# Optimization experiments

Measured on AMD Instinct MI355X. Metric: run time of the kernel, lower is better.

Reference implementation:

```python
import jax, jax.numpy as jnp
import numpy as np

NEG_BIG = -9e15
ALPHA = 0.2  # leaky relu slope

def setup_inputs() -> dict:
    key = jax.random.key(0)
    k1, k2, k3, k4, k5 = jax.random.split(key, 5)
    N, F_in, F_out, H = 4096, 512, 64, 8
    x = jax.random.normal(k1, (N, F_in), dtype=jnp.float32)
    adj = jax.random.randint(k2, (N, N), 0, 2, dtype=jnp.int32)
    W = jax.random.normal(k3, (H, F_in, F_out), dtype=jnp.float32) * (1.414 * (2.0 / (F_in + F_out)) ** 0.5)
    a_source = jax.random.normal(k4, (H, 1, F_out), dtype=jnp.float32) * (1.414 * (2.0 / (1 + F_out)) ** 0.5)
    a_target = jax.random.normal(k5, (H, 1, F_out), dtype=jnp.float32) * (1.414 * (2.0 / (1 + F_out)) ** 0.5)
    return {"x": x, "adj": adj, "W": W, "a_source": a_source, "a_target": a_target}

def reference(x, adj, W, a_source, a_target):
    # Wh: [H, N, F_out]
    Wh = jnp.einsum('nf,hfo->hno', x, W)
    # additive attention logits
    s_i = jnp.sum(a_source * Wh, axis=2, keepdims=True)          # [H, N, 1]
    s_j = jnp.sum(a_target * Wh, axis=2, keepdims=True)          # [H, N, 1]
    e = s_i + jnp.swapaxes(s_j, 1, 2)                            # [H, N, N]
    e = jnp.where(e > 0, e, ALPHA * e)                           # leaky relu
    e = jnp.where(adj[None] > 0, e, jnp.float32(NEG_BIG))        # adjacency mask
    attention = jax.nn.softmax(e, axis=2)                        # [H, N, N]
    h_prime = jnp.einsum('hij,hjo->hio', attention, Wh)          # [H, N, F_out]
    return h_prime
```

## Files before the change

### kernel.cpp

```cpp
#include <hip/hip_runtime.h>
#include <hip/hip_fp16.h>
#include <cstdint>

#define N_NODES 4096
#define F_IN    512
#define F_OUT   64
#define H_HEADS 8
#define JC      4

constexpr float L2E = 1.44269504088896f;

typedef _Float16 half2_t __attribute__((ext_vector_type(2)));
typedef _Float16 half4_t __attribute__((ext_vector_type(4)));
typedef _Float16 half8_t __attribute__((ext_vector_type(8)));
typedef float    f32x4   __attribute__((ext_vector_type(4)));

__device__ inline unsigned int exp2_pk_u(unsigned int au) {
    __half2 h = __builtin_bit_cast(__half2, au);
    h = h2exp2(h);
    return __builtin_bit_cast(unsigned int, h);
}

__global__ __launch_bounds__(256) void k_prep(const int* __restrict__ adj,
                                              const float* __restrict__ W,
                                              unsigned long long* __restrict__ adjwT,
                                              _Float16* __restrict__ wfrag) {
    if (blockIdx.x < 128) {
        int gid = blockIdx.x * 256 + threadIdx.x;
        int h     = gid >> 12;
        int kt    = (gid >> 8) & 15;
        int ntile = (gid >> 6) & 3;
        int lane  = gid & 63;
        int c0 = lane & 15, g = lane >> 4;
        const float* src = W + ((size_t)h * F_IN + kt * 32 + 8 * g) * F_OUT + ntile * 16 + c0;
        half8_t hv;
        #pragma unroll
        for (int t = 0; t < 8; t++) hv[t] = (_Float16)src[(size_t)t * F_OUT];
        *reinterpret_cast<half8_t*>(&wfrag[(size_t)gid * 8]) = hv;
        return;
    }
    int bid  = blockIdx.x - 128;
    int lane = threadIdx.x & 63;
    int wid  = (int)((bid * 256 + threadIdx.x) >> 6);
    int nwaves = (2048 * 256) >> 6;
    const int nchunks = N_NODES * (N_NODES / 64);
    for (int cf = wid; cf < nchunks; cf += nwaves) {
        int v = adj[(size_t)cf * 64 + lane];
        unsigned long long mask = __ballot(v > 0);
        if (lane == 0) {
            int i = cf >> 6, c = cf & 63;
            adjwT[(size_t)c * N_NODES + i] = mask;
        }
    }
}

__global__ __launch_bounds__(512) void k_wh_mfma(const float* __restrict__ x,
                                                 const _Float16* __restrict__ wfrag,
                                                 const float* __restrict__ a_src,
                                                 const float* __restrict__ a_tgt,
                                                 _Float16* __restrict__ WhFrag,
                                                 float* __restrict__ s_iL,
                                                 _Float16* __restrict__ s_jLh) {
    __shared__ f32x4 red[4][4][64];
    const int h    = blockIdx.y;
    const int rt   = blockIdx.x;
    const int t    = threadIdx.x;
    const int lane = t & 63;
    const int w    = t >> 6;
    const int mtw  = w & 3;
    const int kh   = w >> 2;
    const int mt   = rt * 4 + mtw;
    const int c0   = lane & 15;
    const int gl   = lane >> 4;

    f32x4 acc0 = {0.f, 0.f, 0.f, 0.f};
    f32x4 acc1 = {0.f, 0.f, 0.f, 0.f};
    f32x4 acc2 = {0.f, 0.f, 0.f, 0.f};
    f32x4 acc3 = {0.f, 0.f, 0.f, 0.f};

    const float* __restrict__ xr = x + (size_t)(mt * 16 + c0) * F_IN + 8 * gl + kh * 256;
    const _Float16* __restrict__ Bf = wfrag + (size_t)h * (16 * 4 * 512)
                                    + (size_t)kh * 8 * 2048 + (size_t)lane * 8;

    #pragma unroll
    for (int kt = 0; kt < 8; kt++) {
        float4 v0 = *reinterpret_cast<const float4*>(xr + kt * 32);
        float4 v1 = *reinterpret_cast<const float4*>(xr + kt * 32 + 4);
        half8_t a;
        a[0] = (_Float16)v0.x; a[1] = (_Float16)v0.y; a[2] = (_Float16)v0.z; a[3] = (_Float16)v0.w;
        a[4] = (_Float16)v1.x; a[5] = (_Float16)v1.y; a[6] = (_Float16)v1.z; a[7] = (_Float16)v1.w;
        const _Float16* Bk = Bf + (size_t)kt * 2048;
        half8_t b0 = *reinterpret_cast<const half8_t*>(Bk);
        half8_t b1 = *reinterpret_cast<const half8_t*>(Bk + 512);
        half8_t b2 = *reinterpret_cast<const half8_t*>(Bk + 1024);
        half8_t b3 = *reinterpret_cast<const half8_t*>(Bk + 1536);
        acc0 = __builtin_amdgcn_mfma_f32_16x16x32_f16(a, b0, acc0, 0, 0, 0);
        acc1 = __builtin_amdgcn_mfma_f32_16x16x32_f16(a, b1, acc1, 0, 0, 0);
        acc2 = __builtin_amdgcn_mfma_f32_16x16x32_f16(a, b2, acc2, 0, 0, 0);
        acc3 = __builtin_amdgcn_mfma_f32_16x16x32_f16(a, b3, acc3, 0, 0, 0);
    }

    if (kh == 1) {
        red[mtw][0][lane] = acc0;
        red[mtw][1][lane] = acc1;
        red[mtw][2][lane] = acc2;
        red[mtw][3][lane] = acc3;
    }
    __syncthreads();
    if (kh == 1) return;

    acc0 += red[mtw][0][lane];
    acc1 += red[mtw][1][lane];
    acc2 += red[mtw][2][lane];
    acc3 += red[mtw][3][lane];

    const float as0 = a_src[h * 64 + c0],      at0 = a_tgt[h * 64 + c0];
    const float as1 = a_src[h * 64 + 16 + c0], at1 = a_tgt[h * 64 + 16 + c0];
    const float as2 = a_src[h * 64 + 32 + c0], at2 = a_tgt[h * 64 + 32 + c0];
    const float as3 = a_src[h * 64 + 48 + c0], at3 = a_tgt[h * 64 + 48 + c0];

    #pragma unroll
    for (int reg = 0; reg < 4; reg++) {
        float vi = acc0[reg] * as0 + acc1[reg] * as1 + acc2[reg] * as2 + acc3[reg] * as3;
        float vj = acc0[reg] * at0 + acc1[reg] * at1 + acc2[reg] * at2 + acc3[reg] * at3;
        #pragma unroll
        for (int mm = 8; mm >= 1; mm >>= 1) {
            vi += __shfl_xor(vi, mm, 64);
            vj += __shfl_xor(vj, mm, 64);
        }
        if (c0 == 0) {
            int row = mt * 16 + 4 * gl + reg;
            s_iL[h * N_NODES + row]  = vi * L2E;
            s_jLh[h * N_NODES + row] = (_Float16)(vj * L2E);
        }
    }

    const int cc    = mt >> 2;
    const int kb    = (mt >> 1) & 1;
    const int lanep = c0 + 16 * ((mt & 1) * 2 + (gl >> 1));
    const int tb    = 4 * (gl & 1);
    _Float16* dst = WhFrag + (size_t)h * (N_NODES * 64)
                  + (size_t)(cc * 2 + kb) * 2048 + (size_t)lanep * 8 + tb;
    f32x4 accs[4] = {acc0, acc1, acc2, acc3};
    #pragma unroll
    for (int ot = 0; ot < 4; ot++) {
        half4_t hv;
        #pragma unroll
        for (int reg = 0; reg < 4; reg++) hv[reg] = (_Float16)accs[ot][reg];
        *reinterpret_cast<half4_t*>(dst + ot * 512) = hv;
    }
}

__global__ __launch_bounds__(256) void k_hmax(const _Float16* __restrict__ s_jLh,
                                              float* __restrict__ mxAll) {
    __shared__ float red[4];
    const int h = blockIdx.x;
    const int t = threadIdx.x;
    const _Float16* p = s_jLh + h * N_NODES;
    float m = -INFINITY;
    for (int k = t; k < N_NODES; k += 256) m = fmaxf(m, (float)p[k]);
    #pragma unroll
    for (int mm = 32; mm >= 1; mm >>= 1) m = fmaxf(m, __shfl_xor(m, mm, 64));
    if ((t & 63) == 0) red[t >> 6] = m;
    __syncthreads();
    if (t == 0) mxAll[h] = fmaxf(fmaxf(red[0], red[1]), fmaxf(red[2], red[3]));
}

__global__ __launch_bounds__(256) void k_attn_mfma(const _Float16* __restrict__ WhFrag,
                                                   const float* __restrict__ s_iL,
                                                   const float* __restrict__ mxAll,
                                                   const _Float16* __restrict__ s_jLh,
                                                   const unsigned long long* __restrict__ adjwT,
                                                   float* __restrict__ out0,
                                                   _Float16* __restrict__ partH,
                                                   float* __restrict__ lbuf) {
    __shared__ unsigned int ktab[256][4];
    __shared__ _Float16 Bs[2][4096];
    {
        unsigned int bm = threadIdx.x;
        #pragma unroll
        for (int q = 0; q < 4; q++) {
            unsigned int lo = ((bm >> (2 * q)) & 1u) ? 0xFFFFu : 0u;
            unsigned int hi = ((bm >> (2 * q + 1)) & 1u) ? 0xFFFF0000u : 0u;
            ktab[bm][q] = lo | hi;
        }
    }

    const int tid  = threadIdx.x;
    const int h    = blockIdx.y;
    const int jc   = blockIdx.z;
    const int lane = tid & 63;
    const int w    = tid >> 6;
    const int i0   = blockIdx.x * 64 + w * 16;
    const int mrow = lane & 15;
    const int gl   = lane >> 4;
    const int gl8  = gl << 3;

    const float siL = s_iL[h * N_NODES + i0 + mrow];
    const float tmx = siL + mxAll[h];
    const float m   = fmaxf(tmx, 0.2f * tmx);
    const _Float16 uh  = (_Float16)(siL - m);
    const _Float16 n8h = (_Float16)(-0.8f * m);
    half8_t u8, n88, c028;
    #pragma unroll
    for (int q = 0; q < 8; q++) { u8[q] = uh; n88[q] = n8h; c028[q] = (_Float16)0.2f; }

    const _Float16* __restrict__ sjh = s_jLh + h * N_NODES;
    const _Float16* __restrict__ Bh  = WhFrag + (size_t)h * (N_NODES * 64);

    half8_t vone;
    #pragma unroll
    for (int q = 0; q < 8; q++) vone[q] = (_Float16)1.0f;

    f32x4 acc0 = {0.f, 0.f, 0.f, 0.f};
    f32x4 acc1 = {0.f, 0.f, 0.f, 0.f};
    f32x4 acc2 = {0.f, 0.f, 0.f, 0.f};
    f32x4 acc3 = {0.f, 0.f, 0.f, 0.f};
    f32x4 accl = {0.f, 0.f, 0.f, 0.f};

    const int NC   = (N_NODES / 64) / JC;
    const int cbeg = jc * NC;
    const int cend = cbeg + NC;

    {
        const _Float16* src = Bh + (size_t)cbeg * 4096 + tid * 8;
        *reinterpret_cast<half8_t*>(&Bs[0][tid * 8])        = *reinterpret_cast<const half8_t*>(src);
        *reinterpret_cast<half8_t*>(&Bs[0][2048 + tid * 8]) = *reinterpret_cast<const half8_t*>(src + 2048);
    }
    __syncthreads();

    int cur = 0;
    for (int c = cbeg; c < cend; c++) {
        half8_t n0, n1;
        const bool hasNext = (c + 1 < cend);
        if (hasNext) {
            const _Float16* src = Bh + (size_t)(c + 1) * 4096 + tid * 8;
            n0 = *reinterpret_cast<const half8_t*>(src);
            n1 = *reinterpret_cast<const half8_t*>(src + 2048);
        }

        uint2 word = *reinterpret_cast<const uint2*>(&adjwT[(size_t)c * N_NODES + i0 + mrow]);
        #pragma unroll
        for (int kb = 0; kb < 2; kb++) {
            const int jb = c * 64 + kb * 32 + 8 * gl;
            half8_t sjv = *reinterpret_cast<const half8_t*>(&sjh[jb]);
            unsigned int bm8 = ((kb ? word.y : word.x) >> gl8) & 0xFFu;
            uint4 mk = *reinterpret_cast<const uint4*>(&ktab[bm8][0]);

            half8_t a1v = u8 + sjv;
            half8_t a2v = a1v * c028 + n88;
            half8_t amv = __builtin_elementwise_max(a1v, a2v);
            uint4 amu = __builtin_bit_cast(uint4, amv);
            uint4 pu;
            pu.x = exp2_pk_u(amu.x) & mk.x;
            pu.y = exp2_pk_u(amu.y) & mk.y;
            pu.z = exp2_pk_u(amu.z) & mk.z;
            pu.w = exp2_pk_u(amu.w) & mk.w;
            half8_t af = __builtin_bit_cast(half8_t, pu);

            const _Float16* Bk = &Bs[cur][kb * 2048 + lane * 8];
            half8_t b0 = *reinterpret_cast<const half8_t*>(Bk);
            half8_t b1 = *reinterpret_cast<const half8_t*>(Bk + 512);
            half8_t b2 = *reinterpret_cast<const half8_t*>(Bk + 1024);
            half8_t b3 = *reinterpret_cast<const half8_t*>(Bk + 1536);

            acc0 = __builtin_amdgcn_mfma_f32_16x16x32_f16(af, b0, acc0, 0, 0, 0);
            acc1 = __builtin_amdgcn_mfma_f32_16x16x32_f16(af, b1, acc1, 0, 0, 0);
            acc2 = __builtin_amdgcn_mfma_f32_16x16x32_f16(af, b2, acc2, 0, 0, 0);
            acc3 = __builtin_amdgcn_mfma_f32_16x16x32_f16(af, b3, acc3, 0, 0, 0);
            accl = __builtin_amdgcn_mfma_f32_16x16x32_f16(af, vone, accl, 0, 0, 0);
        }

        if (hasNext) {
            *reinterpret_cast<half8_t*>(&Bs[cur ^ 1][tid * 8])        = n0;
            *reinterpret_cast<half8_t*>(&Bs[cur ^ 1][2048 + tid * 8]) = n1;
        }
        __syncthreads();
        cur ^= 1;
    }

    float* lp = lbuf + (size_t)jc * (H_HEADS * N_NODES);
    if (mrow == 0) {
        #pragma unroll
        for (int r = 0; r < 4; r++)
            lp[h * N_NODES + i0 + 4 * gl + r] = accl[r];
    }
    if (jc == 0) {
        #pragma unroll
        for (int r = 0; r < 4; r++) {
            int row   = i0 + 4 * gl + r;
            size_t ob = ((size_t)h * N_NODES + row) * 64 + mrow;
            out0[ob + 0]  = acc0[r];
            out0[ob + 16] = acc1[r];
            out0[ob + 32] = acc2[r];
            out0[ob + 48] = acc3[r];
        }
    } else {
        _Float16* op = partH + (size_t)(jc - 1) * ((size_t)H_HEADS * N_NODES * F_OUT);
        #pragma unroll
        for (int r = 0; r < 4; r++) {
            int row   = i0 + 4 * gl + r;
            size_t ob = ((size_t)h * N_NODES + row) * 64 + mrow;
            op[ob + 0]  = (_Float16)acc0[r];
            op[ob + 16] = (_Float16)acc1[r];
            op[ob + 32] = (_Float16)acc2[r];
            op[ob + 48] = (_Float16)acc3[r];
        }
    }
}

__global__ __launch_bounds__(256) void k_norm(float* __restrict__ out,
                                              const _Float16* __restrict__ partH,
                                              const float* __restrict__ lbuf) {
    const int HN = H_HEADS * N_NODES;
    int idx = blockIdx.x * 256 + threadIdx.x;
    int row = idx >> 4;
    float inv = 1.0f / (lbuf[row] + lbuf[HN + row] + lbuf[2 * HN + row] + lbuf[3 * HN + row]);
    float4 a = reinterpret_cast<const float4*>(out)[idx];
    float s0 = a.x, s1 = a.y, s2 = a.z, s3 = a.w;
    #pragma unroll
    for (int p = 0; p < 3; p++) {
        half4_t hp = *reinterpret_cast<const half4_t*>(
            &partH[(size_t)p * ((size_t)H_HEADS * N_NODES * F_OUT) + (size_t)idx * 4]);
        s0 += (float)hp[0]; s1 += (float)hp[1]; s2 += (float)hp[2]; s3 += (float)hp[3];
    }
    float4 v = {s0 * inv, s1 * inv, s2 * inv, s3 * inv};
    reinterpret_cast<float4*>(out)[idx] = v;
}

extern "C" void kernel_launch(void* const* d_in, const int* in_sizes, int n_in,
                              void* d_out, int out_size, void* d_ws, size_t ws_size,
                              hipStream_t stream) {
    const float* x     = (const float*)d_in[0];
    const int*   adj   = (const int*)d_in[1];
    const float* W     = (const float*)d_in[2];
    const float* a_src = (const float*)d_in[3];
    const float* a_tgt = (const float*)d_in[4];
    float* out = (float*)d_out;

    char* ws = (char*)d_ws;
    size_t off = 0;
    auto alloc = [&](size_t bytes) -> char* {
        char* p = ws + off;
        off += (bytes + 255) & ~(size_t)255;
        return p;
    };
    _Float16* WhFrag = (_Float16*)alloc((size_t)H_HEADS * N_NODES * F_OUT * 2);
    _Float16* wfrag  = (_Float16*)alloc((size_t)H_HEADS * 16 * 4 * 64 * 8 * 2);
    float* s_iL      = (float*)alloc((size_t)H_HEADS * N_NODES * 4);
    _Float16* s_jLh  = (_Float16*)alloc((size_t)H_HEADS * N_NODES * 2);
    float* mxAll     = (float*)alloc((size_t)H_HEADS * 4);
    float* lbuf      = (float*)alloc((size_t)JC * H_HEADS * N_NODES * 4);
    _Float16* partH  = (_Float16*)alloc((size_t)(JC - 1) * H_HEADS * N_NODES * F_OUT * 2);
    unsigned long long* adjwT = (unsigned long long*)alloc((size_t)N_NODES * (N_NODES / 64) * 8);
    (void)ws_size;

    k_prep<<<2176, 256, 0, stream>>>(adj, W, adjwT, wfrag);
    k_wh_mfma<<<dim3(N_NODES / 64, H_HEADS), 512, 0, stream>>>(x, wfrag, a_src, a_tgt,
                                                               WhFrag, s_iL, s_jLh);
    k_hmax<<<H_HEADS, 256, 0, stream>>>(s_jLh, mxAll);
    k_attn_mfma<<<dim3(N_NODES / 64, H_HEADS, JC), 256, 0, stream>>>(WhFrag, s_iL, mxAll, s_jLh,
                                                                     adjwT, out, partH, lbuf);
    k_norm<<<(H_HEADS * N_NODES * F_OUT / 4) / 256, 256, 0, stream>>>(out, partH, lbuf);
}
```

Measured before the change: 82.58 us.

## Process two 16-row tiles per wave in attention kernel to reuse B fragments

Each wave now covers 32 query rows instead of 16. Every shared-memory B fragment load and every s_j load therefore feeds two sets of MFMAs, and the grid is halved in x. This cuts LDS traffic and the per-block staging overhead for each row. The cost is doubled accumulator registers, so a launch_bounds occupancy hint of 4 is added, and there are fewer blocks (1024) to fill the GPU.

```diff
diff --git a/kernel.cpp b/kernel.cpp
--- a/kernel.cpp
+++ b/kernel.cpp
@@ -166,14 +166,14 @@
     if (t == 0) mxAll[h] = fmaxf(fmaxf(red[0], red[1]), fmaxf(red[2], red[3]));
 }
 
-__global__ __launch_bounds__(256) void k_attn_mfma(const _Float16* __restrict__ WhFrag,
-                                                   const float* __restrict__ s_iL,
-                                                   const float* __restrict__ mxAll,
-                                                   const _Float16* __restrict__ s_jLh,
-                                                   const unsigned long long* __restrict__ adjwT,
-                                                   float* __restrict__ out0,
-                                                   _Float16* __restrict__ partH,
-                                                   float* __restrict__ lbuf) {
+__global__ __launch_bounds__(256, 4) void k_attn_mfma(const _Float16* __restrict__ WhFrag,
+                                                      const float* __restrict__ s_iL,
+                                                      const float* __restrict__ mxAll,
+                                                      const _Float16* __restrict__ s_jLh,
+                                                      const unsigned long long* __restrict__ adjwT,
+                                                      float* __restrict__ out0,
+                                                      _Float16* __restrict__ partH,
+                                                      float* __restrict__ lbuf) {
     __shared__ unsigned int ktab[256][4];
     __shared__ _Float16 Bs[2][4096];
     {
@@ -191,19 +191,22 @@
     const int jc   = blockIdx.z;
     const int lane = tid & 63;
     const int w    = tid >> 6;
-    const int i0   = blockIdx.x * 64 + w * 16;
+    const int i0   = blockIdx.x * 128 + w * 32;
     const int mrow = lane & 15;
     const int gl   = lane >> 4;
     const int gl8  = gl << 3;
 
-    const float siL = s_iL[h * N_NODES + i0 + mrow];
-    const float tmx = siL + mxAll[h];
-    const float m   = fmaxf(tmx, 0.2f * tmx);
-    const _Float16 uh  = (_Float16)(siL - m);
-    const _Float16 n8h = (_Float16)(-0.8f * m);
-    half8_t u8, n88, c028;
-    #pragma unroll
-    for (int q = 0; q < 8; q++) { u8[q] = uh; n88[q] = n8h; c028[q] = (_Float16)0.2f; }
+    const float siL0 = s_iL[h * N_NODES + i0 + mrow];
+    const float siL1 = s_iL[h * N_NODES + i0 + 16 + mrow];
+    const float mxh  = mxAll[h];
+    const float tm0 = siL0 + mxh, tm1 = siL1 + mxh;
+    const float m0 = fmaxf(tm0, 0.2f * tm0);
+    const float m1 = fmaxf(tm1, 0.2f * tm1);
+    const half2_t u2_0 = {(_Float16)(siL0 - m0), (_Float16)(siL0 - m0)};
+    const half2_t u2_1 = {(_Float16)(siL1 - m1), (_Float16)(siL1 - m1)};
+    const half2_t n82_0 = {(_Float16)(-0.8f * m0), (_Float16)(-0.8f * m0)};
+    const half2_t n82_1 = {(_Float16)(-0.8f * m1), (_Float16)(-0.8f * m1)};
+    const half2_t c02 = {(_Float16)0.2f, (_Float16)0.2f};
 
     const _Float16* __restrict__ sjh = s_jLh + h * N_NODES;
     const _Float16* __restrict__ Bh  = WhFrag + (size_t)h * (N_NODES * 64);
@@ -212,11 +215,9 @@
     #pragma unroll
     for (int q = 0; q < 8; q++) vone[q] = (_Float16)1.0f;
 
-    f32x4 acc0 = {0.f, 0.f, 0.f, 0.f};
-    f32x4 acc1 = {0.f, 0.f, 0.f, 0.f};
-    f32x4 acc2 = {0.f, 0.f, 0.f, 0.f};
-    f32x4 acc3 = {0.f, 0.f, 0.f, 0.f};
-    f32x4 accl = {0.f, 0.f, 0.f, 0.f};
+    f32x4 accA0 = {0,0,0,0}, accA1 = {0,0,0,0}, accA2 = {0,0,0,0}, accA3 = {0,0,0,0};
+    f32x4 accB0 = {0,0,0,0}, accB1 = {0,0,0,0}, accB2 = {0,0,0,0}, accB3 = {0,0,0,0};
+    f32x4 acclA = {0,0,0,0}, acclB = {0,0,0,0};
 
     const int NC   = (N_NODES / 64) / JC;
     const int cbeg = jc * NC;
@@ -239,36 +240,57 @@
             n1 = *reinterpret_cast<const half8_t*>(src + 2048);
         }
 
-        uint2 word = *reinterpret_cast<const uint2*>(&adjwT[(size_t)c * N_NODES + i0 + mrow]);
+        uint2 word0 = *reinterpret_cast<const uint2*>(&adjwT[(size_t)c * N_NODES + i0 + mrow]);
+        uint2 word1 = *reinterpret_cast<const uint2*>(&adjwT[(size_t)c * N_NODES + i0 + 16 + mrow]);
+
         #pragma unroll
         for (int kb = 0; kb < 2; kb++) {
             const int jb = c * 64 + kb * 32 + 8 * gl;
             half8_t sjv = *reinterpret_cast<const half8_t*>(&sjh[jb]);
-            unsigned int bm8 = ((kb ? word.y : word.x) >> gl8) & 0xFFu;
-            uint4 mk = *reinterpret_cast<const uint4*>(&ktab[bm8][0]);
-
-            half8_t a1v = u8 + sjv;
-            half8_t a2v = a1v * c028 + n88;
-            half8_t amv = __builtin_elementwise_max(a1v, a2v);
-            uint4 amu = __builtin_bit_cast(uint4, amv);
-            uint4 pu;
-            pu.x = exp2_pk_u(amu.x) & mk.x;
-            pu.y = exp2_pk_u(amu.y) & mk.y;
-            pu.z = exp2_pk_u(amu.z) & mk.z;
-            pu.w = exp2_pk_u(amu.w) & mk.w;
-            half8_t af = __builtin_bit_cast(half8_t, pu);
+            unsigned int bm0 = ((kb ? word0.y : word0.x) >> gl8) & 0xFFu;
+            unsigned int bm1 = ((kb ? word1.y : word1.x) >> gl8) & 0xFFu;
+            uint4 mk0 = *reinterpret_cast<const uint4*>(&ktab[bm0][0]);
+            uint4 mk1 = *reinterpret_cast<const uint4*>(&ktab[bm1][0]);
+
+            uint4 sju = __builtin_bit_cast(uint4, sjv);
+            uint4 p0u, p1u;
+            #pragma unroll
+            for (int q = 0; q < 4; q++) {
+                unsigned int sw = (q == 0) ? sju.x : (q == 1) ? sju.y : (q == 2) ? sju.z : sju.w;
+                half2_t sj2 = __builtin_bit_cast(half2_t, sw);
+                half2_t a1 = u2_0 + sj2;
+                half2_t am = __builtin_elementwise_max(a1, a1 * c02 + n82_0);
+                unsigned int pa = exp2_pk_u(__builtin_bit_cast(unsigned int, am));
+                half2_t b1 = u2_1 + sj2;
+                half2_t bm = __builtin_elementwise_max(b1, b1 * c02 + n82_1);
+                unsigned int pb = exp2_pk_u(__builtin_bit_cast(unsigned int, bm));
+                unsigned int ka = (q == 0) ? mk0.x : (q == 1) ? mk0.y : (q == 2) ? mk0.z : mk0.w;
+                unsigned int kbm = (q == 0) ? mk1.x : (q == 1) ? mk1.y : (q == 2) ? mk1.z : mk1.w;
+                pa &= ka; pb &= kbm;
+                if (q == 0) { p0u.x = pa; p1u.x = pb; }
+                else if (q == 1) { p0u.y = pa; p1u.y = pb; }
+                else if (q == 2) { p0u.z = pa; p1u.z = pb; }
+                else { p0u.w = pa; p1u.w = pb; }
+            }
+            half8_t af0 = __builtin_bit_cast(half8_t, p0u);
+            half8_t af1 = __builtin_bit_cast(half8_t, p1u);
 
             const _Float16* Bk = &Bs[cur][kb * 2048 + lane * 8];
             half8_t b0 = *reinterpret_cast<const half8_t*>(Bk);
-            half8_t b1 = *reinterpret_cast<const half8_t*>(Bk + 512);
+            half8_t b1v = *reinterpret_cast<const half8_t*>(Bk + 512);
             half8_t b2 = *reinterpret_cast<const half8_t*>(Bk + 1024);
             half8_t b3 = *reinterpret_cast<const half8_t*>(Bk + 1536);
 
-            acc0 = __builtin_amdgcn_mfma_f32_16x16x32_f16(af, b0, acc0, 0, 0, 0);
-            acc1 = __builtin_amdgcn_mfma_f32_16x16x32_f16(af, b1, acc1, 0, 0, 0);
-            acc2 = __builtin_amdgcn_mfma_f32_16x16x32_f16(af, b2, acc2, 0, 0, 0);
-            acc3 = __builtin_amdgcn_mfma_f32_16x16x32_f16(af, b3, acc3, 0, 0, 0);
-            accl = __builtin_amdgcn_mfma_f32_16x16x32_f16(af, vone, accl, 0, 0, 0);
+            accA0 = __builtin_amdgcn_mfma_f32_16x16x32_f16(af0, b0,  accA0, 0, 0, 0);
+            accB0 = __builtin_amdgcn_mfma_f32_16x16x32_f16(af1, b0,  accB0, 0, 0, 0);
+            accA1 = __builtin_amdgcn_mfma_f32_16x16x32_f16(af0, b1v, accA1, 0, 0, 0);
+            accB1 = __builtin_amdgcn_mfma_f32_16x16x32_f16(af1, b1v, accB1, 0, 0, 0);
+            accA2 = __builtin_amdgcn_mfma_f32_16x16x32_f16(af0, b2,  accA2, 0, 0, 0);
+            accB2 = __builtin_amdgcn_mfma_f32_16x16x32_f16(af1, b2,  accB2, 0, 0, 0);
+            accA3 = __builtin_amdgcn_mfma_f32_16x16x32_f16(af0, b3,  accA3, 0, 0, 0);
+            accB3 = __builtin_amdgcn_mfma_f32_16x16x32_f16(af1, b3,  accB3, 0, 0, 0);
+            acclA = __builtin_amdgcn_mfma_f32_16x16x32_f16(af0, vone, acclA, 0, 0, 0);
+            acclB = __builtin_amdgcn_mfma_f32_16x16x32_f16(af1, vone, acclB, 0, 0, 0);
         }
 
         if (hasNext) {
@@ -282,29 +304,39 @@
     float* lp = lbuf + (size_t)jc * (H_HEADS * N_NODES);
     if (mrow == 0) {
         #pragma unroll
-        for (int r = 0; r < 4; r++)
-            lp[h * N_NODES + i0 + 4 * gl + r] = accl[r];
+        for (int r = 0; r < 4; r++) {
+            lp[h * N_NODES + i0 + 4 * gl + r]      = acclA[r];
+            lp[h * N_NODES + i0 + 16 + 4 * gl + r] = acclB[r];
+        }
     }
     if (jc == 0) {
         #pragma unroll
         for (int r = 0; r < 4; r++) {
-            int row   = i0 + 4 * gl + r;
-            size_t ob = ((size_t)h * N_NODES + row) * 64 + mrow;
-            out0[ob + 0]  = acc0[r];
-            out0[ob + 16] = acc1[r];
-            out0[ob + 32] = acc2[r];
-            out0[ob + 48] = acc3[r];
+            size_t obA = ((size_t)h * N_NODES + i0 + 4 * gl + r) * 64 + mrow;
+            size_t obB = ((size_t)h * N_NODES + i0 + 16 + 4 * gl + r) * 64 + mrow;
+            out0[obA + 0]  = accA0[r];
+            out0[obA + 16] = accA1[r];
+            out0[obA + 32] = accA2[r];
+            out0[obA + 48] = accA3[r];
+            out0[obB + 0]  = accB0[r];
+            out0[obB + 16] = accB1[r];
+            out0[obB + 32] = accB2[r];
+            out0[obB + 48] = accB3[r];
         }
     } else {
         _Float16* op = partH + (size_t)(jc - 1) * ((size_t)H_HEADS * N_NODES * F_OUT);
         #pragma unroll
         for (int r = 0; r < 4; r++) {
-            int row   = i0 + 4 * gl + r;
-            size_t ob = ((size_t)h * N_NODES + row) * 64 + mrow;
-            op[ob + 0]  = (_Float16)acc0[r];
-            op[ob + 16] = (_Float16)acc1[r];
-            op[ob + 32] = (_Float16)acc2[r];
-            op[ob + 48] = (_Float16)acc3[r];
+            size_t obA = ((size_t)h * N_NODES + i0 + 4 * gl + r) * 64 + mrow;
+            size_t obB = ((size_t)h * N_NODES + i0 + 16 + 4 * gl + r) * 64 + mrow;
+            op[obA + 0]  = (_Float16)accA0[r];
+            op[obA + 16] = (_Float16)accA1[r];
+            op[obA + 32] = (_Float16)accA2[r];
+            op[obA + 48] = (_Float16)accA3[r];
+            op[obB + 0]  = (_Float16)accB0[r];
+            op[obB + 16] = (_Float16)accB1[r];
+            op[obB + 32] = (_Float16)accB2[r];
+            op[obB + 48] = (_Float16)accB3[r];
         }
     }
 }
@@ -359,7 +391,7 @@
     k_wh_mfma<<<dim3(N_NODES / 64, H_HEADS), 512, 0, stream>>>(x, wfrag, a_src, a_tgt,
                                                                WhFrag, s_iL, s_jLh);
     k_hmax<<<H_HEADS, 256, 0, stream>>>(s_jLh, mxAll);
-    k_attn_mfma<<<dim3(N_NODES / 64, H_HEADS, JC), 256, 0, stream>>>(WhFrag, s_iL, mxAll, s_jLh,
-                                                                     adjwT, out, partH, lbuf);
+    k_attn_mfma<<<dim3(N_NODES / 128, H_HEADS, JC), 256, 0, stream>>>(WhFrag, s_iL, mxAll, s_jLh,
+                                                                      adjwT, out, partH, lbuf);
     k_norm<<<(H_HEADS * N_NODES * F_OUT / 4) / 256, 256, 0, stream>>>(out, partH, lbuf);
 }
```

Result: faster. 79.23 us (-4.1%).
